# Kernel optimization log

Hardware: AMD Instinct MI355X
Metric: run time of the kernel (lower is better)

Reference implementation:

```python
import jax, jax.numpy as jnp
import numpy as np

N_RES = 320
C_Z = 128
NUM_HEAD = 4
HEAD_DIM = C_Z // NUM_HEAD  # 32
LN_EPS = 1e-5


def layer_norm(x, scale, offset):
    mean = jnp.mean(x, axis=-1, keepdims=True)
    var = jnp.var(x, axis=-1, keepdims=True)
    return (x - mean) * jax.lax.rsqrt(var + LN_EPS) * scale + offset


def setup_inputs() -> dict:
    key = jax.random.key(0)
    ks = jax.random.split(key, 12)
    d = {
        'pair_act': jax.random.normal(ks[0], (N_RES, N_RES, C_Z), jnp.float32),
        'affine_act': jax.random.normal(ks[1], (N_RES, N_RES, C_Z), jnp.float32),
        'pair_mask': jnp.ones((N_RES, N_RES), jnp.float32),
        'pair_ln_scale': jnp.ones((C_Z,), jnp.float32),
        'pair_ln_offset': jnp.zeros((C_Z,), jnp.float32),
        'affine_ln_scale': jnp.ones((C_Z,), jnp.float32),
        'affine_ln_offset': jnp.zeros((C_Z,), jnp.float32),
        'feat_2d_weights': jax.random.normal(ks[2], (C_Z, NUM_HEAD), jnp.float32) / 0.8796256610342398,
        'query_w': jax.random.normal(ks[3], (C_Z, NUM_HEAD, HEAD_DIM), jnp.float32) * 0.05,
        'key_w': jax.random.normal(ks[4], (C_Z, NUM_HEAD, HEAD_DIM), jnp.float32) * 0.05,
        'value_w': jax.random.normal(ks[5], (C_Z, NUM_HEAD, HEAD_DIM), jnp.float32) * 0.05,
        'gating_w': jax.random.normal(ks[6], (C_Z, NUM_HEAD, HEAD_DIM), jnp.float32) * 0.05,
        'output_w': jax.random.normal(ks[7], (NUM_HEAD, HEAD_DIM, C_Z), jnp.float32) * 0.05,
    }
    return d


def reference(pair_act, affine_act, pair_mask,
              pair_ln_scale, pair_ln_offset, affine_ln_scale, affine_ln_offset,
              feat_2d_weights, query_w, key_w, value_w, gating_w, output_w):
    # orientation == 'per_row' -> no swapaxes
    pair_ln = layer_norm(pair_act, pair_ln_scale, pair_ln_offset)          # [N,N,c]
    affine_ln = layer_norm(affine_act, affine_ln_scale, affine_ln_offset)  # [N,N,c]

    # padding bias [N,1,1,N]
    bias = (1e9 * (pair_mask - 1.0))[:, None, None, :]
    # nonbatched pair bias [H,N,N]
    nonbatched_bias = jnp.einsum('qkc,ch->hqk', affine_ln, feat_2d_weights)

    # attention (q_data == m_data == pair_ln)
    scale = HEAD_DIM ** (-0.5)
    q = jnp.einsum('bqa,ahc->bqhc', pair_ln, query_w) * scale
    k = jnp.einsum('bka,ahc->bkhc', pair_ln, key_w)
    v = jnp.einsum('bka,ahc->bkhc', pair_ln, value_w)

    logits = jnp.einsum('bqhc,bkhc->bhqk', q, k) + bias + nonbatched_bias[None]
    weights = jax.nn.softmax(logits, axis=-1)
    weighted_avg = jnp.einsum('bhqk,bkhc->bqhc', weights, v)

    gate = jax.nn.sigmoid(jnp.einsum('bqc,chv->bqhv', pair_ln, gating_w))
    weighted_avg = weighted_avg * gate

    out = jnp.einsum('bqhc,hco->bqo', weighted_avg, output_w)  # [N,N,c_z]
    return out
```

## Files before the change

kernel.cpp:

```cpp
#include <hip/hip_runtime.h>
#include <hip/hip_bf16.h>

#define N_RES 320
#define C_Z   128
#define NH    4
#define HD    32
#define M_TOT (N_RES*N_RES)
#define LN_EPS 1e-5f
#define QSCALE 0.17677669529663687f
#define LOG2E  1.4426950408889634f

typedef __attribute__((ext_vector_type(8))) short short8;
typedef __attribute__((ext_vector_type(4))) float floatx4;
typedef __attribute__((ext_vector_type(4))) unsigned uintx4;

#define OFF_MASK 0
#define OFF_PLS  102400
#define OFF_PLO  102528
#define OFF_ALS  102656
#define OFF_ALO  102784
#define OFF_FWT  102912
#define OFF_WQT  104960
#define OFF_WKT  121344
#define OFF_WVT  137728
#define OFF_WGT  154112
#define OFF_WOT  170496
#define ARENA_N  186880

__device__ __forceinline__ float u16_to_f(unsigned short s){
    union { unsigned u; float f; } v; v.u = ((unsigned)s) << 16; return v.f;
}
__device__ __forceinline__ unsigned short bf16r(float f){
    union { __hip_bfloat16 b; unsigned short s; } v; v.b = __float2bfloat16(f); return v.s;
}
__device__ __forceinline__ unsigned pack2(float a, float b){
    return (unsigned)bf16r(a) | ((unsigned)bf16r(b) << 16);
}
__device__ __forceinline__ float ld_dual(const void* s, size_t i, bool isbf){
    return isbf ? u16_to_f(((const unsigned short*)s)[i]) : ((const float*)s)[i];
}

__device__ __forceinline__ short8 xpose_frag(unsigned A0, unsigned A1,
                                             unsigned B0, unsigned B1, int lane)
{
#if __has_builtin(__builtin_amdgcn_permlane32_swap) && __has_builtin(__builtin_amdgcn_permlane16_swap)
    (void)lane;
    auto uv0 = __builtin_amdgcn_permlane32_swap(A0, B0, false, false);
    auto uv1 = __builtin_amdgcn_permlane32_swap(A1, B1, false, false);
    auto t02 = __builtin_amdgcn_permlane16_swap(uv0[0], uv0[1], false, false);
    auto t13 = __builtin_amdgcn_permlane16_swap(uv1[0], uv1[1], false, false);
    uintx4 u = { t02[0], t13[0], t02[1], t13[1] };
#else
    bool hi32 = lane >= 32, oddq = (lane & 16) != 0;
    unsigned A0x = __shfl_xor(A0, 32, 64), B0x = __shfl_xor(B0, 32, 64);
    unsigned A1x = __shfl_xor(A1, 32, 64), B1x = __shfl_xor(B1, 32, 64);
    unsigned U0 = hi32 ? B0x : A0, V0 = hi32 ? B0 : A0x;
    unsigned U1 = hi32 ? B1x : A1, V1 = hi32 ? B1 : A1x;
    unsigned U0x = __shfl_xor(U0, 16, 64), V0x = __shfl_xor(V0, 16, 64);
    unsigned U1x = __shfl_xor(U1, 16, 64), V1x = __shfl_xor(V1, 16, 64);
    unsigned T0 = oddq ? V0x : U0, T2 = oddq ? V0 : U0x;
    unsigned T1 = oddq ? V1x : U1, T3 = oddq ? V1 : U1x;
    uintx4 u = { T0, T1, T2, T3 };
#endif
    union { uintx4 u; short8 s; } cvt; cvt.u = u;
    return cvt.s;
}

__global__ __launch_bounds__(256) void k_conv_all(
    const void* __restrict__ s_mask, const void* __restrict__ s_pls,
    const void* __restrict__ s_plo,  const void* __restrict__ s_als,
    const void* __restrict__ s_alo,  const void* __restrict__ s_fw,
    const void* __restrict__ s_wq,   const void* __restrict__ s_wk,
    const void* __restrict__ s_wv,   const void* __restrict__ s_wg,
    const void* __restrict__ s_wo,
    unsigned short* __restrict__ arena, const unsigned* __restrict__ probe)
{
    int gid = blockIdx.x * 256 + threadIdx.x;
    bool isbf = (probe[0] & 0xffffu) != 0;
    float val;
    if (gid < OFF_PLS)      val = ld_dual(s_mask, gid, isbf);
    else if (gid < OFF_PLO) val = ld_dual(s_pls, gid - OFF_PLS, isbf);
    else if (gid < OFF_ALS) val = ld_dual(s_plo, gid - OFF_PLO, isbf);
    else if (gid < OFF_ALO) val = ld_dual(s_als, gid - OFF_ALS, isbf);
    else if (gid < OFF_FWT) val = ld_dual(s_alo, gid - OFF_ALO, isbf);
    else if (gid < OFF_WQT){
        int local = gid - OFF_FWT, hh = local >> 7, c = local & 127;
        val = (hh < 4) ? ld_dual(s_fw, c*NH + hh, isbf) : 0.0f;
    } else if (gid < OFF_WOT){
        int seg = (gid - OFF_WQT) >> 14;
        int local = (gid - OFF_WQT) & 16383;
        int hc = local >> 7, z = local & 127;
        const void* src = (seg == 0) ? s_wq : (seg == 1) ? s_wk : (seg == 2) ? s_wv : s_wg;
        val = ld_dual(src, z*128 + hc, isbf);
    } else {
        int local = gid - OFF_WOT, o = local >> 7, hc = local & 127;
        val = ld_dual(s_wo, hc*128 + o, isbf);
    }
    arena[gid] = bf16r(val);
}

__global__ __launch_bounds__(256) void k_ln_fused(
    const void* __restrict__ pair, const void* __restrict__ affine,
    const unsigned short* __restrict__ pls, const unsigned short* __restrict__ plo,
    const unsigned short* __restrict__ als, const unsigned short* __restrict__ alo,
    const unsigned short* __restrict__ fwpT,
    unsigned short* __restrict__ pl, float* __restrict__ nb,
    const unsigned* __restrict__ probe)
{
    int bid = blockIdx.x;
    bool isPair = bid < 1600;
    int tid = threadIdx.x, lane = tid & 63, wave = tid >> 6;
    int c16 = lane & 15, quad = lane >> 4, rb = quad * 4;
    int m0 = (isPair ? bid : bid - 1600) * 64 + wave * 16;
    bool isbf = (probe[0] & 0xffffu) != 0;

    const void* src = isPair ? pair : affine;
    const unsigned short* sc = isPair ? pls : als;
    const unsigned short* of = isPair ? plo : alo;

    float x[32];
    if (isbf){
        const short8* a8 = (const short8*)src;
        #pragma unroll
        for (int ks = 0; ks < 4; ++ks){
            short8 t = a8[(size_t)(m0 + c16)*16 + ks*4 + quad];
            #pragma unroll
            for (int j = 0; j < 8; ++j) x[ks*8+j] = u16_to_f((unsigned short)t[j]);
        }
    } else {
        const floatx4* a4 = (const floatx4*)src;
        #pragma unroll
        for (int ks = 0; ks < 4; ++ks){
            floatx4 f0 = a4[(size_t)(m0 + c16)*32 + ks*8 + quad*2];
            floatx4 f1 = a4[(size_t)(m0 + c16)*32 + ks*8 + quad*2 + 1];
            #pragma unroll
            for (int j = 0; j < 4; ++j){ x[ks*8+j] = f0[j]; x[ks*8+4+j] = f1[j]; }
        }
    }
    float s = 0.f, ss = 0.f;
    #pragma unroll
    for (int j = 0; j < 32; ++j){ s += x[j]; ss += x[j]*x[j]; }
    s  += __shfl_xor(s, 16, 64);  s  += __shfl_xor(s, 32, 64);
    ss += __shfl_xor(ss, 16, 64); ss += __shfl_xor(ss, 32, 64);
    float mean = s * (1.0f/128.0f);
    float var  = ss * (1.0f/128.0f) - mean*mean;
    float rs   = rsqrtf(var + LN_EPS);

    const short8* sc8 = (const short8*)sc;
    const short8* of8 = (const short8*)of;

    if (isPair){
        short8* pl8 = (short8*)pl;
        #pragma unroll
        for (int ks = 0; ks < 4; ++ks){
            short8 scv = sc8[ks*4 + quad], ofv = of8[ks*4 + quad];
            short8 lf;
            #pragma unroll
            for (int j = 0; j < 8; ++j){
                float l = (x[ks*8+j] - mean) * rs * u16_to_f((unsigned short)scv[j])
                        + u16_to_f((unsigned short)ofv[j]);
                lf[j] = (short)bf16r(l);
            }
            pl8[(size_t)(m0 + c16)*16 + ks*4 + quad] = lf;
        }
    } else {
        short8 lf[4], lg[4];
        #pragma unroll
        for (int ks = 0; ks < 4; ++ks){
            short8 scv = sc8[ks*4 + quad], ofv = of8[ks*4 + quad];
            #pragma unroll
            for (int j = 0; j < 8; ++j){
                float l = (x[ks*8+j] - mean) * rs * u16_to_f((unsigned short)scv[j])
                        + u16_to_f((unsigned short)ofv[j]);
                unsigned short hi = bf16r(l);
                lf[ks][j] = (short)hi;
                lg[ks][j] = (short)bf16r(l - u16_to_f(hi));
            }
        }
        floatx4 acc = {0.f, 0.f, 0.f, 0.f};
        const short8* fw8 = (const short8*)fwpT;
        #pragma unroll
        for (int ks = 0; ks < 4; ++ks){
            short8 fwf = fw8[c16*16 + ks*4 + quad];
            acc = __builtin_amdgcn_mfma_f32_16x16x32_bf16(lf[ks], fwf, acc, 0, 0, 0);
            acc = __builtin_amdgcn_mfma_f32_16x16x32_bf16(lg[ks], fwf, acc, 0, 0, 0);
        }
        acc = acc * LOG2E;
        if (c16 < 4)
            *(floatx4*)&nb[(size_t)c16 * M_TOT + m0 + rb] = acc;
    }
}

__global__ __launch_bounds__(256) void k_nbmax(float* __restrict__ nb)
{
    int tid = threadIdx.x, lane = tid & 63, wave = tid >> 6;
    int row = blockIdx.x * 4 + wave;
    float* r = nb + (size_t)row * N_RES;
    floatx4 v = *(const floatx4*)&r[lane*4];
    float x5 = r[256 + lane];
    float m = fmaxf(fmaxf(v[0], v[1]), fmaxf(v[2], v[3]));
    m = fmaxf(m, x5);
    #pragma unroll
    for (int d = 32; d; d >>= 1) m = fmaxf(m, __shfl_xor(m, d, 64));
    float M = m + 8.0f;
    floatx4 vo = { v[0]-M, v[1]-M, v[2]-M, v[3]-M };
    *(floatx4*)&r[lane*4] = vo;
    r[256 + lane] = x5 - M;
}

__global__ __launch_bounds__(640, 4) void k_attn(
    const unsigned short* __restrict__ pl,
    const unsigned short* __restrict__ wqT, const unsigned short* __restrict__ wkT,
    const unsigned short* __restrict__ wvT, const unsigned short* __restrict__ wgT,
    const unsigned short* __restrict__ maskc, const float* __restrict__ nb,
    unsigned short* __restrict__ wab)
{
    __shared__ __align__(16) unsigned short Ks[320*40];
    __shared__ __align__(16) unsigned short Vt[32*328];
    __shared__ __align__(16) float biasl[320];

    int b = blockIdx.x, h = blockIdx.y;
    int tid = threadIdx.x, lane = tid & 63, wave = tid >> 6;
    int c16 = lane & 15, quad = lane >> 4, rb = quad * 4;

    const short8* plrow8 = (const short8*)(pl + (size_t)b * N_RES * C_Z);
    const short8* Ks8 = (const short8*)Ks;
    const short8* Vt8 = (const short8*)Vt;
    const short8* wqT8 = (const short8*)wqT;
    const short8* wkT8 = (const short8*)wkT;
    const short8* wvT8 = (const short8*)wvT;
    const short8* wgT8 = (const short8*)wgT;
    floatx4 Z = {0.f, 0.f, 0.f, 0.f};

    if (tid < 320)
        biasl[tid] = (LOG2E * 1e9f) * (u16_to_f(maskc[(size_t)b * N_RES + tid]) - 1.0f);

    #pragma unroll 1
    for (int mt = wave; mt < 20; mt += 10){
        short8 a[4];
        #pragma unroll
        for (int ks = 0; ks < 4; ++ks)
            a[ks] = plrow8[(mt*16 + c16)*16 + ks*4 + quad];

        #pragma unroll
        for (int ct = 0; ct < 2; ++ct){
            int hc = h*HD + ct*16 + c16;
            floatx4 acc = Z;
            #pragma unroll
            for (int ks = 0; ks < 4; ++ks){
                short8 bw = wkT8[hc*16 + ks*4 + quad];
                acc = __builtin_amdgcn_mfma_f32_16x16x32_bf16(a[ks], bw, acc, 0, 0, 0);
            }
            #pragma unroll
            for (int i = 0; i < 4; ++i)
                Ks[(mt*16 + rb + i)*40 + ct*16 + c16] = bf16r(acc[i]);
        }
        #pragma unroll
        for (int ct = 0; ct < 2; ++ct){
            int hc = h*HD + ct*16 + c16;
            floatx4 acc = Z;
            #pragma unroll
            for (int ks = 0; ks < 4; ++ks){
                short8 bw = wvT8[hc*16 + ks*4 + quad];
                acc = __builtin_amdgcn_mfma_f32_16x16x32_bf16(bw, a[ks], acc, 0, 0, 0);
            }
            #pragma unroll
            for (int i = 0; i < 4; ++i)
                Vt[(ct*16 + rb + i)*328 + mt*16 + c16] = bf16r(acc[i]);
        }
    }
    __syncthreads();

    #pragma unroll 1
    for (int mt = wave; mt < 20; mt += 10){
        int m0 = mt * 16;
        short8 plf[4];
        #pragma unroll
        for (int ks = 0; ks < 4; ++ks)
            plf[ks] = plrow8[(m0 + c16)*16 + ks*4 + quad];

        floatx4 q0 = Z, q1 = Z, g0v = Z, g1v = Z;
        #pragma unroll
        for (int ks = 0; ks < 4; ++ks){
            short8 w0 = wqT8[(h*HD + c16)*16 + ks*4 + quad];
            short8 w1 = wqT8[(h*HD + 16 + c16)*16 + ks*4 + quad];
            q0 = __builtin_amdgcn_mfma_f32_16x16x32_bf16(w0, plf[ks], q0, 0, 0, 0);
            q1 = __builtin_amdgcn_mfma_f32_16x16x32_bf16(w1, plf[ks], q1, 0, 0, 0);
            short8 u0 = wgT8[(h*HD + c16)*16 + ks*4 + quad];
            short8 u1 = wgT8[(h*HD + 16 + c16)*16 + ks*4 + quad];
            g0v = __builtin_amdgcn_mfma_f32_16x16x32_bf16(u0, plf[ks], g0v, 0, 0, 0);
            g1v = __builtin_amdgcn_mfma_f32_16x16x32_bf16(u1, plf[ks], g1v, 0, 0, 0);
        }
        const float QS = QSCALE * LOG2E;
        short8 qf = xpose_frag(pack2(q0[0]*QS, q0[1]*QS), pack2(q0[2]*QS, q0[3]*QS),
                               pack2(q1[0]*QS, q1[1]*QS), pack2(q1[2]*QS, q1[3]*QS), lane);

        float lpart = 0.f;
        floatx4 acc0 = Z, acc1 = Z;
        const float* nbq = nb + (size_t)h * M_TOT + (size_t)(m0 + c16) * N_RES;

        #pragma unroll 2
        for (int kt2 = 0; kt2 < 10; ++kt2){
            int k0 = kt2 * 32;
            short8 kfa = Ks8[(k0 + c16)*5 + quad];
            short8 kfb = Ks8[(k0 + 16 + c16)*5 + quad];
            floatx4 sa = __builtin_amdgcn_mfma_f32_16x16x32_bf16(kfa, qf, Z, 0, 0, 0);
            floatx4 sb = __builtin_amdgcn_mfma_f32_16x16x32_bf16(kfb, qf, Z, 0, 0, 0);
            floatx4 nba = *(const floatx4*)&nbq[k0 + rb];
            floatx4 nbb = *(const floatx4*)&nbq[k0 + 16 + rb];
            floatx4 bia = *(const floatx4*)&biasl[k0 + rb];
            floatx4 bib = *(const floatx4*)&biasl[k0 + 16 + rb];
            float pa[4], pb[4], ts = 0.f;
            #pragma unroll
            for (int i = 0; i < 4; ++i){
                pa[i] = exp2f(sa[i] + nba[i] + bia[i]);
                pb[i] = exp2f(sb[i] + nbb[i] + bib[i]);
                ts += pa[i] + pb[i];
            }
            lpart += ts;
            short8 pt = xpose_frag(pack2(pa[0], pa[1]), pack2(pa[2], pa[3]),
                                   pack2(pb[0], pb[1]), pack2(pb[2], pb[3]), lane);
            short8 v0 = Vt8[c16*41 + kt2*4 + quad];
            short8 v1 = Vt8[(16 + c16)*41 + kt2*4 + quad];
            acc0 = __builtin_amdgcn_mfma_f32_16x16x32_bf16(v0, pt, acc0, 0, 0, 0);
            acc1 = __builtin_amdgcn_mfma_f32_16x16x32_bf16(v1, pt, acc1, 0, 0, 0);
        }

        lpart += __shfl_xor(lpart, 16, 64);
        lpart += __shfl_xor(lpart, 32, 64);
        float inv = 1.0f / lpart;
        float o[8];
        #pragma unroll
        for (int i = 0; i < 4; ++i){
            o[i]     = acc0[i] * inv * (1.0f/(1.0f + __expf(-g0v[i])));
            o[4 + i] = acc1[i] * inv * (1.0f/(1.0f + __expf(-g1v[i])));
        }
        size_t base = (size_t)h * (M_TOT*HD) + (size_t)(b*N_RES + m0 + c16) * HD;
        uint2 s0 = { pack2(o[0], o[1]), pack2(o[2], o[3]) };
        uint2 s1 = { pack2(o[4], o[5]), pack2(o[6], o[7]) };
        *(uint2*)&wab[base + rb]      = s0;
        *(uint2*)&wab[base + 16 + rb] = s1;
    }
}

__global__ __launch_bounds__(256, 4) void k_outproj(
    const unsigned short* __restrict__ wab, const unsigned short* __restrict__ woT,
    void* __restrict__ out, const unsigned* __restrict__ probe)
{
    int tid = threadIdx.x, lane = tid & 63, wave = tid >> 6;
    int c16 = lane & 15, quad = lane >> 4, rb = quad * 4;
    int m0 = blockIdx.x * 64 + wave * 16;
    bool isbf = (probe[0] & 0xffffu) != 0;

    const short8* wab8 = (const short8*)wab;
    const short8* woT8 = (const short8*)woT;
    floatx4 Z = {0.f, 0.f, 0.f, 0.f};

    short8 a[4];
    #pragma unroll
    for (int ks = 0; ks < 4; ++ks)
        a[ks] = wab8[(size_t)ks * (M_TOT*4) + (size_t)(m0 + c16)*4 + quad];

    #pragma unroll 1
    for (int nt = 0; nt < 8; ++nt){
        floatx4 acc = Z;
        #pragma unroll
        for (int ks = 0; ks < 4; ++ks){
            short8 bf = woT8[(nt*16 + c16)*16 + ks*4 + quad];
            acc = __builtin_amdgcn_mfma_f32_16x16x32_bf16(a[ks], bf, acc, 0, 0, 0);
        }
        #pragma unroll
        for (int i = 0; i < 4; ++i){
            size_t idx = (size_t)(m0 + rb + i)*C_Z + nt*16 + c16;
            if (isbf) ((unsigned short*)out)[idx] = bf16r(acc[i]);
            else      ((float*)out)[idx] = acc[i];
        }
    }
}

extern "C" void kernel_launch(void* const* d_in, const int* in_sizes, int n_in,
                              void* d_out, int out_size, void* d_ws, size_t ws_size,
                              hipStream_t stream)
{
    const unsigned* probe = (const unsigned*)d_in[3];

    char* w = (char*)d_ws;
    unsigned short* arena = (unsigned short*)w;
    unsigned short* mask_c = arena + OFF_MASK;
    unsigned short* pls_c  = arena + OFF_PLS;
    unsigned short* plo_c  = arena + OFF_PLO;
    unsigned short* als_c  = arena + OFF_ALS;
    unsigned short* alo_c  = arena + OFF_ALO;
    unsigned short* fwT_c  = arena + OFF_FWT;
    unsigned short* wqT_c  = arena + OFF_WQT;
    unsigned short* wkT_c  = arena + OFF_WKT;
    unsigned short* wvT_c  = arena + OFF_WVT;
    unsigned short* wgT_c  = arena + OFF_WGT;
    unsigned short* woT_c  = arena + OFF_WOT;
    float*          nb     = (float*)(w + 524288);
    unsigned short* pl     = (unsigned short*)(w + 2162688);
    unsigned short* wab    = (unsigned short*)(w + 28377088);

    k_conv_all<<<730, 256, 0, stream>>>(d_in[2], d_in[3], d_in[4], d_in[5], d_in[6],
                                        d_in[7], d_in[8], d_in[9], d_in[10], d_in[11],
                                        d_in[12], arena, probe);
    k_ln_fused<<<3200, 256, 0, stream>>>(d_in[0], d_in[1], pls_c, plo_c, als_c, alo_c,
                                         fwT_c, pl, nb, probe);
    k_nbmax   <<<320, 256, 0, stream>>>(nb);
    k_attn    <<<dim3(N_RES, NH), 640, 0, stream>>>(pl, wqT_c, wkT_c, wvT_c, wgT_c,
                                                    mask_c, nb, wab);
    k_outproj <<<1600, 256, 0, stream>>>(wab, woT_c, d_out, probe);
}
```

Measured before the change: 358.1 us.

## Split K/V projection into separate kernel and parallelize attention over query tiles

Moves the per-row K and V projection out of the attention kernel into a new k_kv kernel that writes K and transposed V to global memory. The attention kernel then launches with a third grid dimension over query tiles and smaller 256-thread blocks, reading K/V from global memory instead of LDS. The mask bias is precomputed in k_nbmax. This gives more independent blocks and drops the in-kernel barrier. In exchange it adds a global round trip of about 50 MB for K and V and an extra kernel launch.

```diff
diff --git a/kernel.cpp b/kernel.cpp
--- a/kernel.cpp
+++ b/kernel.cpp
@@ -191,7 +191,9 @@
     }
 }
 
-__global__ __launch_bounds__(256) void k_nbmax(float* __restrict__ nb)
+__global__ __launch_bounds__(256) void k_nbmax(
+    float* __restrict__ nb, const unsigned short* __restrict__ maskc,
+    float* __restrict__ biasf)
 {
     int tid = threadIdx.x, lane = tid & 63, wave = tid >> 6;
     int row = blockIdx.x * 4 + wave;
@@ -206,42 +208,35 @@
     floatx4 vo = { v[0]-M, v[1]-M, v[2]-M, v[3]-M };
     *(floatx4*)&r[lane*4] = vo;
     r[256 + lane] = x5 - M;
-}
-
-__global__ __launch_bounds__(640, 4) void k_attn(
+
+    int b = blockIdx.x;
+    for (int idx = tid; idx < N_RES; idx += 256)
+        biasf[(size_t)b*N_RES + idx] =
+            (LOG2E * 1e9f) * (u16_to_f(maskc[(size_t)b*N_RES + idx]) - 1.0f);
+}
+
+__global__ __launch_bounds__(256, 4) void k_kv(
     const unsigned short* __restrict__ pl,
-    const unsigned short* __restrict__ wqT, const unsigned short* __restrict__ wkT,
-    const unsigned short* __restrict__ wvT, const unsigned short* __restrict__ wgT,
-    const unsigned short* __restrict__ maskc, const float* __restrict__ nb,
-    unsigned short* __restrict__ wab)
-{
-    __shared__ __align__(16) unsigned short Ks[320*40];
-    __shared__ __align__(16) unsigned short Vt[32*328];
-    __shared__ __align__(16) float biasl[320];
-
-    int b = blockIdx.x, h = blockIdx.y;
+    const unsigned short* __restrict__ wkT, const unsigned short* __restrict__ wvT,
+    unsigned short* __restrict__ Kb, unsigned short* __restrict__ VTb)
+{
     int tid = threadIdx.x, lane = tid & 63, wave = tid >> 6;
     int c16 = lane & 15, quad = lane >> 4, rb = quad * 4;
+    int b = blockIdx.x / 5, mt = (blockIdx.x % 5) * 4 + wave;
 
     const short8* plrow8 = (const short8*)(pl + (size_t)b * N_RES * C_Z);
-    const short8* Ks8 = (const short8*)Ks;
-    const short8* Vt8 = (const short8*)Vt;
-    const short8* wqT8 = (const short8*)wqT;
     const short8* wkT8 = (const short8*)wkT;
     const short8* wvT8 = (const short8*)wvT;
-    const short8* wgT8 = (const short8*)wgT;
     floatx4 Z = {0.f, 0.f, 0.f, 0.f};
 
-    if (tid < 320)
-        biasl[tid] = (LOG2E * 1e9f) * (u16_to_f(maskc[(size_t)b * N_RES + tid]) - 1.0f);
+    short8 a[4];
+    #pragma unroll
+    for (int ks = 0; ks < 4; ++ks)
+        a[ks] = plrow8[(mt*16 + c16)*16 + ks*4 + quad];
 
     #pragma unroll 1
-    for (int mt = wave; mt < 20; mt += 10){
-        short8 a[4];
-        #pragma unroll
-        for (int ks = 0; ks < 4; ++ks)
-            a[ks] = plrow8[(mt*16 + c16)*16 + ks*4 + quad];
-
+    for (int h = 0; h < NH; ++h){
+        size_t bh = (size_t)(b*NH + h);
         #pragma unroll
         for (int ct = 0; ct < 2; ++ct){
             int hc = h*HD + ct*16 + c16;
@@ -253,7 +248,7 @@
             }
             #pragma unroll
             for (int i = 0; i < 4; ++i)
-                Ks[(mt*16 + rb + i)*40 + ct*16 + c16] = bf16r(acc[i]);
+                Kb[(bh*N_RES + mt*16 + rb + i)*HD + ct*16 + c16] = bf16r(acc[i]);
         }
         #pragma unroll
         for (int ct = 0; ct < 2; ++ct){
@@ -266,81 +261,98 @@
             }
             #pragma unroll
             for (int i = 0; i < 4; ++i)
-                Vt[(ct*16 + rb + i)*328 + mt*16 + c16] = bf16r(acc[i]);
-        }
-    }
-    __syncthreads();
-
-    #pragma unroll 1
-    for (int mt = wave; mt < 20; mt += 10){
-        int m0 = mt * 16;
-        short8 plf[4];
-        #pragma unroll
-        for (int ks = 0; ks < 4; ++ks)
-            plf[ks] = plrow8[(m0 + c16)*16 + ks*4 + quad];
-
-        floatx4 q0 = Z, q1 = Z, g0v = Z, g1v = Z;
-        #pragma unroll
-        for (int ks = 0; ks < 4; ++ks){
-            short8 w0 = wqT8[(h*HD + c16)*16 + ks*4 + quad];
-            short8 w1 = wqT8[(h*HD + 16 + c16)*16 + ks*4 + quad];
-            q0 = __builtin_amdgcn_mfma_f32_16x16x32_bf16(w0, plf[ks], q0, 0, 0, 0);
-            q1 = __builtin_amdgcn_mfma_f32_16x16x32_bf16(w1, plf[ks], q1, 0, 0, 0);
-            short8 u0 = wgT8[(h*HD + c16)*16 + ks*4 + quad];
-            short8 u1 = wgT8[(h*HD + 16 + c16)*16 + ks*4 + quad];
-            g0v = __builtin_amdgcn_mfma_f32_16x16x32_bf16(u0, plf[ks], g0v, 0, 0, 0);
-            g1v = __builtin_amdgcn_mfma_f32_16x16x32_bf16(u1, plf[ks], g1v, 0, 0, 0);
-        }
-        const float QS = QSCALE * LOG2E;
-        short8 qf = xpose_frag(pack2(q0[0]*QS, q0[1]*QS), pack2(q0[2]*QS, q0[3]*QS),
-                               pack2(q1[0]*QS, q1[1]*QS), pack2(q1[2]*QS, q1[3]*QS), lane);
-
-        float lpart = 0.f;
-        floatx4 acc0 = Z, acc1 = Z;
-        const float* nbq = nb + (size_t)h * M_TOT + (size_t)(m0 + c16) * N_RES;
-
-        #pragma unroll 2
-        for (int kt2 = 0; kt2 < 10; ++kt2){
-            int k0 = kt2 * 32;
-            short8 kfa = Ks8[(k0 + c16)*5 + quad];
-            short8 kfb = Ks8[(k0 + 16 + c16)*5 + quad];
-            floatx4 sa = __builtin_amdgcn_mfma_f32_16x16x32_bf16(kfa, qf, Z, 0, 0, 0);
-            floatx4 sb = __builtin_amdgcn_mfma_f32_16x16x32_bf16(kfb, qf, Z, 0, 0, 0);
-            floatx4 nba = *(const floatx4*)&nbq[k0 + rb];
-            floatx4 nbb = *(const floatx4*)&nbq[k0 + 16 + rb];
-            floatx4 bia = *(const floatx4*)&biasl[k0 + rb];
-            floatx4 bib = *(const floatx4*)&biasl[k0 + 16 + rb];
-            float pa[4], pb[4], ts = 0.f;
-            #pragma unroll
-            for (int i = 0; i < 4; ++i){
-                pa[i] = exp2f(sa[i] + nba[i] + bia[i]);
-                pb[i] = exp2f(sb[i] + nbb[i] + bib[i]);
-                ts += pa[i] + pb[i];
-            }
-            lpart += ts;
-            short8 pt = xpose_frag(pack2(pa[0], pa[1]), pack2(pa[2], pa[3]),
-                                   pack2(pb[0], pb[1]), pack2(pb[2], pb[3]), lane);
-            short8 v0 = Vt8[c16*41 + kt2*4 + quad];
-            short8 v1 = Vt8[(16 + c16)*41 + kt2*4 + quad];
-            acc0 = __builtin_amdgcn_mfma_f32_16x16x32_bf16(v0, pt, acc0, 0, 0, 0);
-            acc1 = __builtin_amdgcn_mfma_f32_16x16x32_bf16(v1, pt, acc1, 0, 0, 0);
-        }
-
-        lpart += __shfl_xor(lpart, 16, 64);
-        lpart += __shfl_xor(lpart, 32, 64);
-        float inv = 1.0f / lpart;
-        float o[8];
+                VTb[(bh*HD + ct*16 + rb + i)*N_RES + mt*16 + c16] = bf16r(acc[i]);
+        }
+    }
+}
+
+__global__ __launch_bounds__(256, 4) void k_attn(
+    const unsigned short* __restrict__ pl,
+    const unsigned short* __restrict__ wqT, const unsigned short* __restrict__ wgT,
+    const unsigned short* __restrict__ Kb, const unsigned short* __restrict__ VTb,
+    const float* __restrict__ nb, const float* __restrict__ biasf,
+    unsigned short* __restrict__ wab)
+{
+    int b = blockIdx.x, h = blockIdx.y;
+    int tid = threadIdx.x, lane = tid & 63, wave = tid >> 6;
+    int c16 = lane & 15, quad = lane >> 4, rb = quad * 4;
+    int mt = blockIdx.z * 4 + wave, m0 = mt * 16;
+    size_t bh = (size_t)(b*NH + h);
+
+    const short8* plrow8 = (const short8*)(pl + (size_t)b * N_RES * C_Z);
+    const short8* Kb8 = (const short8*)(Kb + bh * N_RES * HD);
+    const short8* VT8 = (const short8*)(VTb + bh * HD * N_RES);
+    const short8* wqT8 = (const short8*)wqT;
+    const short8* wgT8 = (const short8*)wgT;
+    floatx4 Z = {0.f, 0.f, 0.f, 0.f};
+
+    short8 plf[4];
+    #pragma unroll
+    for (int ks = 0; ks < 4; ++ks)
+        plf[ks] = plrow8[(m0 + c16)*16 + ks*4 + quad];
+
+    floatx4 q0 = Z, q1 = Z, g0v = Z, g1v = Z;
+    #pragma unroll
+    for (int ks = 0; ks < 4; ++ks){
+        short8 w0 = wqT8[(h*HD + c16)*16 + ks*4 + quad];
+        short8 w1 = wqT8[(h*HD + 16 + c16)*16 + ks*4 + quad];
+        q0 = __builtin_amdgcn_mfma_f32_16x16x32_bf16(w0, plf[ks], q0, 0, 0, 0);
+        q1 = __builtin_amdgcn_mfma_f32_16x16x32_bf16(w1, plf[ks], q1, 0, 0, 0);
+        short8 u0 = wgT8[(h*HD + c16)*16 + ks*4 + quad];
+        short8 u1 = wgT8[(h*HD + 16 + c16)*16 + ks*4 + quad];
+        g0v = __builtin_amdgcn_mfma_f32_16x16x32_bf16(u0, plf[ks], g0v, 0, 0, 0);
+        g1v = __builtin_amdgcn_mfma_f32_16x16x32_bf16(u1, plf[ks], g1v, 0, 0, 0);
+    }
+    const float QS = QSCALE * LOG2E;
+    short8 qf = xpose_frag(pack2(q0[0]*QS, q0[1]*QS), pack2(q0[2]*QS, q0[3]*QS),
+                           pack2(q1[0]*QS, q1[1]*QS), pack2(q1[2]*QS, q1[3]*QS), lane);
+
+    float lpart = 0.f;
+    floatx4 acc0 = Z, acc1 = Z;
+    const float* nbq = nb + (size_t)h * M_TOT + (size_t)(m0 + c16) * N_RES;
+    const float* bfq = biasf + (size_t)b * N_RES;
+
+    #pragma unroll 2
+    for (int kt2 = 0; kt2 < 10; ++kt2){
+        int k0 = kt2 * 32;
+        short8 kfa = Kb8[(k0 + c16)*4 + quad];
+        short8 kfb = Kb8[(k0 + 16 + c16)*4 + quad];
+        floatx4 sa = __builtin_amdgcn_mfma_f32_16x16x32_bf16(kfa, qf, Z, 0, 0, 0);
+        floatx4 sb = __builtin_amdgcn_mfma_f32_16x16x32_bf16(kfb, qf, Z, 0, 0, 0);
+        floatx4 nba = *(const floatx4*)&nbq[k0 + rb];
+        floatx4 nbb = *(const floatx4*)&nbq[k0 + 16 + rb];
+        floatx4 bia = *(const floatx4*)&bfq[k0 + rb];
+        floatx4 bib = *(const floatx4*)&bfq[k0 + 16 + rb];
+        float pa[4], pb[4], ts = 0.f;
         #pragma unroll
         for (int i = 0; i < 4; ++i){
-            o[i]     = acc0[i] * inv * (1.0f/(1.0f + __expf(-g0v[i])));
-            o[4 + i] = acc1[i] * inv * (1.0f/(1.0f + __expf(-g1v[i])));
-        }
-        size_t base = (size_t)h * (M_TOT*HD) + (size_t)(b*N_RES + m0 + c16) * HD;
-        uint2 s0 = { pack2(o[0], o[1]), pack2(o[2], o[3]) };
-        uint2 s1 = { pack2(o[4], o[5]), pack2(o[6], o[7]) };
-        *(uint2*)&wab[base + rb]      = s0;
-        *(uint2*)&wab[base + 16 + rb] = s1;
-    }
+            pa[i] = exp2f(sa[i] + nba[i] + bia[i]);
+            pb[i] = exp2f(sb[i] + nbb[i] + bib[i]);
+            ts += pa[i] + pb[i];
+        }
+        lpart += ts;
+        short8 pt = xpose_frag(pack2(pa[0], pa[1]), pack2(pa[2], pa[3]),
+                               pack2(pb[0], pb[1]), pack2(pb[2], pb[3]), lane);
+        short8 v0 = VT8[c16*40 + kt2*4 + quad];
+        short8 v1 = VT8[(16 + c16)*40 + kt2*4 + quad];
+        acc0 = __builtin_amdgcn_mfma_f32_16x16x32_bf16(v0, pt, acc0, 0, 0, 0);
+        acc1 = __builtin_amdgcn_mfma_f32_16x16x32_bf16(v1, pt, acc1, 0, 0, 0);
+    }
+
+    lpart += __shfl_xor(lpart, 16, 64);
+    lpart += __shfl_xor(lpart, 32, 64);
+    float inv = 1.0f / lpart;
+    float o[8];
+    #pragma unroll
+    for (int i = 0; i < 4; ++i){
+        o[i]     = acc0[i] * inv * (1.0f/(1.0f + __expf(-g0v[i])));
+        o[4 + i] = acc1[i] * inv * (1.0f/(1.0f + __expf(-g1v[i])));
+    }
+    size_t base = (size_t)h * (M_TOT*HD) + (size_t)(b*N_RES + m0 + c16) * HD;
+    uint2 s0 = { pack2(o[0], o[1]), pack2(o[2], o[3]) };
+    uint2 s1 = { pack2(o[4], o[5]), pack2(o[6], o[7]) };
+    *(uint2*)&wab[base + rb]      = s0;
+    *(uint2*)&wab[base + 16 + rb] = s1;
 }
 
 __global__ __launch_bounds__(256, 4) void k_outproj(
@@ -400,14 +412,18 @@
     float*          nb     = (float*)(w + 524288);
     unsigned short* pl     = (unsigned short*)(w + 2162688);
     unsigned short* wab    = (unsigned short*)(w + 28377088);
+    float*          biasf  = (float*)(w + 54591488);
+    unsigned short* Kbuf   = (unsigned short*)(w + 55001088);
+    unsigned short* VTbuf  = (unsigned short*)(w + 81215488);
 
     k_conv_all<<<730, 256, 0, stream>>>(d_in[2], d_in[3], d_in[4], d_in[5], d_in[6],
                                         d_in[7], d_in[8], d_in[9], d_in[10], d_in[11],
                                         d_in[12], arena, probe);
     k_ln_fused<<<3200, 256, 0, stream>>>(d_in[0], d_in[1], pls_c, plo_c, als_c, alo_c,
                                          fwT_c, pl, nb, probe);
-    k_nbmax   <<<320, 256, 0, stream>>>(nb);
-    k_attn    <<<dim3(N_RES, NH), 640, 0, stream>>>(pl, wqT_c, wkT_c, wvT_c, wgT_c,
-                                                    mask_c, nb, wab);
+    k_nbmax   <<<320, 256, 0, stream>>>(nb, mask_c, biasf);
+    k_kv      <<<1600, 256, 0, stream>>>(pl, wkT_c, wvT_c, Kbuf, VTbuf);
+    k_attn    <<<dim3(N_RES, NH, 5), 256, 0, stream>>>(pl, wqT_c, wgT_c, Kbuf, VTbuf,
+                                                       nb, biasf, wab);
     k_outproj <<<1600, 256, 0, stream>>>(wab, woT_c, d_out, probe);
 }
```

Measured after the change: 473.2 us. 32.2% more time.

## Process two query tiles per wave to share K/V fragment loads

Applied to the files above, without the earlier changes.

Each wave now handles both of its query tiles together in a single key loop instead of looping over them one at a time. The K and V LDS fragment loads and bias loads are reused across the two tiles, and the two MFMA chains give more independent work to interleave. The gating projection is moved after the attention loop so its accumulators are not live during it. This raises register pressure and the unroll of the key loop drops to 1, which may reduce occupancy or scheduling freedom.

```diff
diff --git a/kernel.cpp b/kernel.cpp
--- a/kernel.cpp
+++ b/kernel.cpp
@@ -271,75 +271,107 @@
     }
     __syncthreads();
 
-    #pragma unroll 1
-    for (int mt = wave; mt < 20; mt += 10){
-        int m0 = mt * 16;
-        short8 plf[4];
-        #pragma unroll
-        for (int ks = 0; ks < 4; ++ks)
-            plf[ks] = plrow8[(m0 + c16)*16 + ks*4 + quad];
-
-        floatx4 q0 = Z, q1 = Z, g0v = Z, g1v = Z;
-        #pragma unroll
-        for (int ks = 0; ks < 4; ++ks){
-            short8 w0 = wqT8[(h*HD + c16)*16 + ks*4 + quad];
-            short8 w1 = wqT8[(h*HD + 16 + c16)*16 + ks*4 + quad];
-            q0 = __builtin_amdgcn_mfma_f32_16x16x32_bf16(w0, plf[ks], q0, 0, 0, 0);
-            q1 = __builtin_amdgcn_mfma_f32_16x16x32_bf16(w1, plf[ks], q1, 0, 0, 0);
-            short8 u0 = wgT8[(h*HD + c16)*16 + ks*4 + quad];
-            short8 u1 = wgT8[(h*HD + 16 + c16)*16 + ks*4 + quad];
-            g0v = __builtin_amdgcn_mfma_f32_16x16x32_bf16(u0, plf[ks], g0v, 0, 0, 0);
-            g1v = __builtin_amdgcn_mfma_f32_16x16x32_bf16(u1, plf[ks], g1v, 0, 0, 0);
-        }
-        const float QS = QSCALE * LOG2E;
-        short8 qf = xpose_frag(pack2(q0[0]*QS, q0[1]*QS), pack2(q0[2]*QS, q0[3]*QS),
-                               pack2(q1[0]*QS, q1[1]*QS), pack2(q1[2]*QS, q1[3]*QS), lane);
-
-        float lpart = 0.f;
-        floatx4 acc0 = Z, acc1 = Z;
-        const float* nbq = nb + (size_t)h * M_TOT + (size_t)(m0 + c16) * N_RES;
-
-        #pragma unroll 2
+    {
+        int m0A = wave * 16, m0B = (wave + 10) * 16;
+
+        short8 qfA, qfB;
+        {
+            floatx4 qa0 = Z, qa1 = Z, qb0 = Z, qb1 = Z;
+            #pragma unroll
+            for (int ks = 0; ks < 4; ++ks){
+                short8 plA = plrow8[(m0A + c16)*16 + ks*4 + quad];
+                short8 plB = plrow8[(m0B + c16)*16 + ks*4 + quad];
+                short8 w0 = wqT8[(h*HD + c16)*16 + ks*4 + quad];
+                short8 w1 = wqT8[(h*HD + 16 + c16)*16 + ks*4 + quad];
+                qa0 = __builtin_amdgcn_mfma_f32_16x16x32_bf16(w0, plA, qa0, 0, 0, 0);
+                qa1 = __builtin_amdgcn_mfma_f32_16x16x32_bf16(w1, plA, qa1, 0, 0, 0);
+                qb0 = __builtin_amdgcn_mfma_f32_16x16x32_bf16(w0, plB, qb0, 0, 0, 0);
+                qb1 = __builtin_amdgcn_mfma_f32_16x16x32_bf16(w1, plB, qb1, 0, 0, 0);
+            }
+            const float QS = QSCALE * LOG2E;
+            qfA = xpose_frag(pack2(qa0[0]*QS, qa0[1]*QS), pack2(qa0[2]*QS, qa0[3]*QS),
+                             pack2(qa1[0]*QS, qa1[1]*QS), pack2(qa1[2]*QS, qa1[3]*QS), lane);
+            qfB = xpose_frag(pack2(qb0[0]*QS, qb0[1]*QS), pack2(qb0[2]*QS, qb0[3]*QS),
+                             pack2(qb1[0]*QS, qb1[1]*QS), pack2(qb1[2]*QS, qb1[3]*QS), lane);
+        }
+
+        float lA = 0.f, lB = 0.f;
+        floatx4 a0A = Z, a1A = Z, a0B = Z, a1B = Z;
+        const float* nbqA = nb + (size_t)h * M_TOT + (size_t)(m0A + c16) * N_RES;
+        const float* nbqB = nb + (size_t)h * M_TOT + (size_t)(m0B + c16) * N_RES;
+
+        #pragma unroll 1
         for (int kt2 = 0; kt2 < 10; ++kt2){
             int k0 = kt2 * 32;
             short8 kfa = Ks8[(k0 + c16)*5 + quad];
             short8 kfb = Ks8[(k0 + 16 + c16)*5 + quad];
-            floatx4 sa = __builtin_amdgcn_mfma_f32_16x16x32_bf16(kfa, qf, Z, 0, 0, 0);
-            floatx4 sb = __builtin_amdgcn_mfma_f32_16x16x32_bf16(kfb, qf, Z, 0, 0, 0);
-            floatx4 nba = *(const floatx4*)&nbq[k0 + rb];
-            floatx4 nbb = *(const floatx4*)&nbq[k0 + 16 + rb];
+            floatx4 saA = __builtin_amdgcn_mfma_f32_16x16x32_bf16(kfa, qfA, Z, 0, 0, 0);
+            floatx4 sbA = __builtin_amdgcn_mfma_f32_16x16x32_bf16(kfb, qfA, Z, 0, 0, 0);
+            floatx4 saB = __builtin_amdgcn_mfma_f32_16x16x32_bf16(kfa, qfB, Z, 0, 0, 0);
+            floatx4 sbB = __builtin_amdgcn_mfma_f32_16x16x32_bf16(kfb, qfB, Z, 0, 0, 0);
             floatx4 bia = *(const floatx4*)&biasl[k0 + rb];
             floatx4 bib = *(const floatx4*)&biasl[k0 + 16 + rb];
-            float pa[4], pb[4], ts = 0.f;
+            floatx4 nbaA = *(const floatx4*)&nbqA[k0 + rb];
+            floatx4 nbbA = *(const floatx4*)&nbqA[k0 + 16 + rb];
+            floatx4 nbaB = *(const floatx4*)&nbqB[k0 + rb];
+            floatx4 nbbB = *(const floatx4*)&nbqB[k0 + 16 + rb];
+            float paA[4], pbA[4], paB[4], pbB[4], tsA = 0.f, tsB = 0.f;
             #pragma unroll
             for (int i = 0; i < 4; ++i){
-                pa[i] = exp2f(sa[i] + nba[i] + bia[i]);
-                pb[i] = exp2f(sb[i] + nbb[i] + bib[i]);
-                ts += pa[i] + pb[i];
-            }
-            lpart += ts;
-            short8 pt = xpose_frag(pack2(pa[0], pa[1]), pack2(pa[2], pa[3]),
-                                   pack2(pb[0], pb[1]), pack2(pb[2], pb[3]), lane);
+                paA[i] = exp2f(saA[i] + nbaA[i] + bia[i]);
+                pbA[i] = exp2f(sbA[i] + nbbA[i] + bib[i]);
+                paB[i] = exp2f(saB[i] + nbaB[i] + bia[i]);
+                pbB[i] = exp2f(sbB[i] + nbbB[i] + bib[i]);
+                tsA += paA[i] + pbA[i];
+                tsB += paB[i] + pbB[i];
+            }
+            lA += tsA;  lB += tsB;
+            short8 ptA = xpose_frag(pack2(paA[0], paA[1]), pack2(paA[2], paA[3]),
+                                    pack2(pbA[0], pbA[1]), pack2(pbA[2], pbA[3]), lane);
+            short8 ptB = xpose_frag(pack2(paB[0], paB[1]), pack2(paB[2], paB[3]),
+                                    pack2(pbB[0], pbB[1]), pack2(pbB[2], pbB[3]), lane);
             short8 v0 = Vt8[c16*41 + kt2*4 + quad];
             short8 v1 = Vt8[(16 + c16)*41 + kt2*4 + quad];
-            acc0 = __builtin_amdgcn_mfma_f32_16x16x32_bf16(v0, pt, acc0, 0, 0, 0);
-            acc1 = __builtin_amdgcn_mfma_f32_16x16x32_bf16(v1, pt, acc1, 0, 0, 0);
-        }
-
-        lpart += __shfl_xor(lpart, 16, 64);
-        lpart += __shfl_xor(lpart, 32, 64);
-        float inv = 1.0f / lpart;
-        float o[8];
+            a0A = __builtin_amdgcn_mfma_f32_16x16x32_bf16(v0, ptA, a0A, 0, 0, 0);
+            a1A = __builtin_amdgcn_mfma_f32_16x16x32_bf16(v1, ptA, a1A, 0, 0, 0);
+            a0B = __builtin_amdgcn_mfma_f32_16x16x32_bf16(v0, ptB, a0B, 0, 0, 0);
+            a1B = __builtin_amdgcn_mfma_f32_16x16x32_bf16(v1, ptB, a1B, 0, 0, 0);
+        }
+
+        lA += __shfl_xor(lA, 16, 64);  lA += __shfl_xor(lA, 32, 64);
+        lB += __shfl_xor(lB, 16, 64);  lB += __shfl_xor(lB, 32, 64);
+        float invA = 1.0f / lA, invB = 1.0f / lB;
+
+        floatx4 g0A = Z, g1A = Z, g0B = Z, g1B = Z;
+        #pragma unroll
+        for (int ks = 0; ks < 4; ++ks){
+            short8 plA = plrow8[(m0A + c16)*16 + ks*4 + quad];
+            short8 plB = plrow8[(m0B + c16)*16 + ks*4 + quad];
+            short8 u0 = wgT8[(h*HD + c16)*16 + ks*4 + quad];
+            short8 u1 = wgT8[(h*HD + 16 + c16)*16 + ks*4 + quad];
+            g0A = __builtin_amdgcn_mfma_f32_16x16x32_bf16(u0, plA, g0A, 0, 0, 0);
+            g1A = __builtin_amdgcn_mfma_f32_16x16x32_bf16(u1, plA, g1A, 0, 0, 0);
+            g0B = __builtin_amdgcn_mfma_f32_16x16x32_bf16(u0, plB, g0B, 0, 0, 0);
+            g1B = __builtin_amdgcn_mfma_f32_16x16x32_bf16(u1, plB, g1B, 0, 0, 0);
+        }
+        float oA[8], oB[8];
         #pragma unroll
         for (int i = 0; i < 4; ++i){
-            o[i]     = acc0[i] * inv * (1.0f/(1.0f + __expf(-g0v[i])));
-            o[4 + i] = acc1[i] * inv * (1.0f/(1.0f + __expf(-g1v[i])));
-        }
-        size_t base = (size_t)h * (M_TOT*HD) + (size_t)(b*N_RES + m0 + c16) * HD;
-        uint2 s0 = { pack2(o[0], o[1]), pack2(o[2], o[3]) };
-        uint2 s1 = { pack2(o[4], o[5]), pack2(o[6], o[7]) };
-        *(uint2*)&wab[base + rb]      = s0;
-        *(uint2*)&wab[base + 16 + rb] = s1;
+            oA[i]     = a0A[i] * invA * (1.0f/(1.0f + __expf(-g0A[i])));
+            oA[4 + i] = a1A[i] * invA * (1.0f/(1.0f + __expf(-g1A[i])));
+            oB[i]     = a0B[i] * invB * (1.0f/(1.0f + __expf(-g0B[i])));
+            oB[4 + i] = a1B[i] * invB * (1.0f/(1.0f + __expf(-g1B[i])));
+        }
+        size_t baseA = (size_t)h * (M_TOT*HD) + (size_t)(b*N_RES + m0A + c16) * HD;
+        size_t baseB = (size_t)h * (M_TOT*HD) + (size_t)(b*N_RES + m0B + c16) * HD;
+        uint2 sA0 = { pack2(oA[0], oA[1]), pack2(oA[2], oA[3]) };
+        uint2 sA1 = { pack2(oA[4], oA[5]), pack2(oA[6], oA[7]) };
+        uint2 sB0 = { pack2(oB[0], oB[1]), pack2(oB[2], oB[3]) };
+        uint2 sB1 = { pack2(oB[4], oB[5]), pack2(oB[6], oB[7]) };
+        *(uint2*)&wab[baseA + rb]      = sA0;
+        *(uint2*)&wab[baseA + 16 + rb] = sA1;
+        *(uint2*)&wab[baseB + rb]      = sB0;
+        *(uint2*)&wab[baseB + 16 + rb] = sB1;
     }
 }
 
```

Result: faster. 348.0 us (-2.8%).
